# Kernel tuning notes

Measured on AMD Instinct MI355X. Metric: run time of the kernel, lower is better.

## Reference

```python
import jax, jax.numpy as jnp
import numpy as np

NUM_CAMS, BS, NUM_QUERY, MAX_LEN, EMBED_DIMS, NPTS = 6, 1, 40000, 10000, 256, 4


def setup_inputs() -> dict:
    key = jax.random.key(0)
    kq, kr, km = jax.random.split(key, 3)
    query = jax.random.normal(kq, (BS, NUM_QUERY, EMBED_DIMS), dtype=jnp.float32)
    reference_points_cam = jax.random.normal(
        kr, (NUM_CAMS, BS, NUM_QUERY, NPTS, 2), dtype=jnp.float32)
    bev_mask = jax.random.randint(km, (NUM_CAMS, BS, NUM_QUERY, NPTS), 0, 2).astype(jnp.int32)
    return {"query": query, "reference_points_cam": reference_points_cam, "bev_mask": bev_mask}


def reference(query, reference_points_cam, bev_mask):
    # valid[c, q]: query q is seen by camera c (any of the NPTS mask bits set); bs == 1
    valid = (bev_mask > 0).any(-1)            # (cams, bs, Q) bool
    valid0 = valid[:, 0]                      # (cams, Q)

    # Stable stream compaction: valid indices first, in ascending query order.
    order = jnp.argsort(~valid0, axis=-1, stable=True)      # (cams, Q)
    indexes = order[:, :MAX_LEN].astype(jnp.int32)          # (cams, max_len)
    indexes_len = jnp.minimum(valid0.sum(-1), MAX_LEN).astype(jnp.int32)  # (cams,)

    # Padded gather/rebatch; zero out slots beyond each camera's valid count.
    pos_ok = jnp.arange(MAX_LEN)[None, :] < indexes_len[:, None]          # (cams, max_len)
    queries_rebatch = query[0][indexes]                                   # (cams, max_len, E)
    queries_rebatch = jnp.where(pos_ok[:, :, None], queries_rebatch, 0.0)

    ref0 = reference_points_cam[:, 0]                                     # (cams, Q, NPTS, 2)
    reference_points_rebatch = jax.vmap(lambda r, i: r[i])(ref0, indexes) # (cams, max_len, NPTS, 2)
    reference_points_rebatch = jnp.where(
        pos_ok[:, :, None, None], reference_points_rebatch, 0.0)

    # count_norm: 1 / (number of cameras that see each query, clamped to >= 1)
    count = valid.astype(jnp.float32).sum(0)                 # (bs, Q)
    count_norm = (1.0 / jnp.maximum(count, 1.0))[..., None]  # (bs, Q, 1)

    return (indexes,
            indexes_len,
            queries_rebatch.reshape(BS * NUM_CAMS, MAX_LEN, EMBED_DIMS),
            reference_points_rebatch.reshape(BS * NUM_CAMS, MAX_LEN, NPTS, 2),
            count_norm)
```

## Files before the change

kernel.cpp:

```cpp
#include <hip/hip_runtime.h>
#include <hip/hip_bf16.h>

#define NUM_CAMS 6
#define NQ       40000
#define MAX_LEN  10000
#define ED       256
#define NBLK     ((NQ + 255) / 256)

typedef float f32x2 __attribute__((ext_vector_type(2)));

#define OFF_IDX  0
#define OFF_LEN  (NUM_CAMS * MAX_LEN)
#define OFF_Q    (OFF_LEN + NUM_CAMS)
#define OFF_REF  (OFF_Q + NUM_CAMS * MAX_LEN * ED)
#define OFF_CNT  (OFF_REF + NUM_CAMS * MAX_LEN * 8)

#define WS_OFF 0
#define WS_TOT (NUM_CAMS * NBLK)
#define WS_LEN (WS_TOT + NUM_CAMS)
#define WS_POS (WS_LEN + NUM_CAMS + 6)
#define WS_NEED_BYTES ((WS_POS + NUM_CAMS * NQ) * 4)

#define QBLOCKS      (NQ / 4)
#define TAIL_BLOCKS  (NUM_CAMS * MAX_LEN / 4)
#define CNT_BLOCKS   ((NQ + 255) / 256)
#define GATHER_BLOCKS (NUM_CAMS * MAX_LEN / 4)

__global__ void kA_counts(const int* __restrict__ bev, float* __restrict__ out,
                          int* __restrict__ ws) {
    __shared__ int cnt[NUM_CAMS];
    const int tid = threadIdx.x;
    const int blk = blockIdx.x;
    const int q   = blk * 256 + tid;
    if (tid < NUM_CAMS) cnt[tid] = 0;
    __syncthreads();
    const int lane = tid & 63;
    const bool inb = q < NQ;
    int myCount = 0;
    #pragma unroll
    for (int cam = 0; cam < NUM_CAMS; ++cam) {
        bool v = false;
        if (inb) {
            const int4 m = *reinterpret_cast<const int4*>(bev + ((size_t)cam * NQ + q) * 4);
            v = (m.x > 0) | (m.y > 0) | (m.z > 0) | (m.w > 0);
        }
        myCount += v ? 1 : 0;
        unsigned long long bal = __ballot(v);
        if (lane == 0) atomicAdd(&cnt[cam], __popcll(bal));
    }
    if (inb) out[OFF_CNT + q] = 1.0f / fmaxf((float)myCount, 1.0f);
    __syncthreads();
    if (tid < NUM_CAMS) ws[WS_OFF + tid * NBLK + blk] = cnt[tid];
}

__global__ void kB_scan(float* __restrict__ out, int* __restrict__ ws) {
    const int cam  = blockIdx.x;
    const int lane = threadIdx.x;
    int running = 0;
    for (int base = 0; base < NBLK; base += 64) {
        const int i = base + lane;
        int val = (i < NBLK) ? ws[WS_OFF + cam * NBLK + i] : 0;
        int v = val;
        for (int d = 1; d < 64; d <<= 1) {
            int n = __shfl_up(v, d, 64);
            if (lane >= d) v += n;
        }
        if (i < NBLK) ws[WS_OFF + cam * NBLK + i] = v - val + running;
        running += __shfl(v, 63, 64);
    }
    if (lane == 0) {
        ws[WS_TOT + cam] = running;
        const int len = running < MAX_LEN ? running : MAX_LEN;
        ws[WS_LEN + cam] = len;
        out[OFF_LEN + cam] = (float)len;
    }
}

__global__ void kC_indexes(const int* __restrict__ bev, float* __restrict__ out,
                           int* __restrict__ ws, int usePos) {
    const int blk = blockIdx.x;
    const int cam = blockIdx.y;
    const int tid = threadIdx.x;
    const int q    = blk * 256 + tid;
    const int lane = tid & 63;
    const int wave = tid >> 6;
    const bool inb = q < NQ;
    bool v = false;
    if (inb) {
        const int4 m = *reinterpret_cast<const int4*>(bev + ((size_t)cam * NQ + q) * 4);
        v = (m.x > 0) | (m.y > 0) | (m.z > 0) | (m.w > 0);
    }
    const unsigned long long bal = __ballot(v);
    __shared__ int waveSums[4];
    if (lane == 0) waveSums[wave] = __popcll(bal);
    __syncthreads();
    int waveOff = 0;
    #pragma unroll
    for (int w = 0; w < 4; ++w)
        if (w < wave) waveOff += waveSums[w];
    const int prefix   = __popcll(bal & ((1ull << lane) - 1ull));
    const int blockOff = ws[WS_OFF + cam * NBLK + blk];
    const int total    = ws[WS_TOT + cam];
    if (inb) {
        const int vb  = blockOff + waveOff + prefix;
        const int pos = v ? vb : (total + (q - vb));
        if (pos < MAX_LEN) out[OFF_IDX + cam * MAX_LEN + pos] = (float)q;
        if (usePos) ws[WS_POS + cam * NQ + q] = (v && vb < MAX_LEN) ? vb : -1;
    }
}

__global__ void kGatherQ(const float* __restrict__ query, const float* __restrict__ refp,
                         float* __restrict__ out, const int* __restrict__ ws) {
    const int blk   = blockIdx.x;
    const int tid   = threadIdx.x;
    const int group = tid >> 6;
    const int lane  = tid & 63;
    if (blk >= QBLOCKS) {
        const int rowId = (blk - QBLOCKS) * 4 + group;
        const int cam   = rowId / MAX_LEN;
        const int j     = rowId - cam * MAX_LEN;
        if (j < ws[WS_LEN + cam]) return;
        const f32x2 z = (f32x2)(0.f);
        f32x2* o2 = reinterpret_cast<f32x2*>(out + OFF_Q + (size_t)rowId * ED + lane * 4);
        o2[0] = z; o2[1] = z;
        if (lane < 4)
            *reinterpret_cast<f32x2*>(out + OFF_REF + (size_t)rowId * 8 + lane * 2) = z;
        return;
    }
    const int q = blk * 4 + group;

    int pos[NUM_CAMS];
    bool any = false;
    #pragma unroll
    for (int cam = 0; cam < NUM_CAMS; ++cam) {
        const int p = ws[WS_POS + cam * NQ + q];
        pos[cam] = p;
        any |= (p >= 0);
    }
    if (!any) return;

    const float4 vq = *reinterpret_cast<const float4*>(query + (size_t)q * ED + lane * 4);
    f32x2 a; a.x = vq.x; a.y = vq.y;
    f32x2 b; b.x = vq.z; b.y = vq.w;

    #pragma unroll
    for (int cam = 0; cam < NUM_CAMS; ++cam) {
        const int p = pos[cam];
        if (p >= 0) {
            f32x2* o2 = reinterpret_cast<f32x2*>(out + OFF_Q + ((size_t)cam * MAX_LEN + p) * ED + lane * 4);
            __builtin_nontemporal_store(a, o2);
            __builtin_nontemporal_store(b, o2 + 1);
            if (lane < 4) {
                const f32x2 r = *reinterpret_cast<const f32x2*>(refp + ((size_t)cam * NQ + q) * 8 + lane * 2);
                *reinterpret_cast<f32x2*>(out + OFF_REF + ((size_t)cam * MAX_LEN + p) * 8 + lane * 2) = r;
            }
        }
    }
}

__global__ void kGather(const float* __restrict__ query, const float* __restrict__ refp,
                        float* __restrict__ out, const int* __restrict__ ws,
                        const int* __restrict__ bev) {
    const int blk = blockIdx.x;
    const int tid = threadIdx.x;
    if (blk >= GATHER_BLOCKS) {
        const int q = (blk - GATHER_BLOCKS) * 256 + tid;
        if (q < NQ) {
            int cnt = 0;
            #pragma unroll
            for (int cam = 0; cam < NUM_CAMS; ++cam) {
                const int4 m = *reinterpret_cast<const int4*>(bev + ((size_t)cam * NQ + q) * 4);
                cnt += ((m.x > 0) | (m.y > 0) | (m.z > 0) | (m.w > 0)) ? 1 : 0;
            }
            out[OFF_CNT + q] = 1.0f / fmaxf((float)cnt, 1.0f);
        }
        return;
    }
    const int rowId = blk * 4 + (tid >> 6);
    const int lane  = tid & 63;
    const int cam   = rowId / MAX_LEN;
    const int j     = rowId - cam * MAX_LEN;
    const int len   = ws[WS_LEN + cam];

    f32x2 a = (f32x2)(0.f), b = (f32x2)(0.f), r0 = (f32x2)(0.f), r1 = (f32x2)(0.f);
    if (j < len) {
        const int idx = (int)out[OFF_IDX + cam * MAX_LEN + j];
        const float4 vq = *reinterpret_cast<const float4*>(query + (size_t)idx * ED + lane * 4);
        a.x = vq.x; a.y = vq.y;
        b.x = vq.z; b.y = vq.w;
        if (lane < 2) {
            const float4 r = *reinterpret_cast<const float4*>(refp + ((size_t)cam * NQ + idx) * 8 + lane * 4);
            r0.x = r.x; r0.y = r.y;
            r1.x = r.z; r1.y = r.w;
        }
    }
    f32x2* o2 = reinterpret_cast<f32x2*>(out + OFF_Q + (size_t)rowId * ED + lane * 4);
    __builtin_nontemporal_store(a, o2);
    __builtin_nontemporal_store(b, o2 + 1);
    if (lane < 2) {
        f32x2* r2 = reinterpret_cast<f32x2*>(out + OFF_REF + (size_t)rowId * 8 + lane * 4);
        r2[0] = r0;
        r2[1] = r1;
    }
}

extern "C" void kernel_launch(void* const* d_in, const int* in_sizes, int n_in,
                              void* d_out, int out_size, void* d_ws, size_t ws_size,
                              hipStream_t stream) {
    const float* query = (const float*)d_in[0];
    const float* refp  = (const float*)d_in[1];
    const int*   bev   = (const int*)d_in[2];
    float* out = (float*)d_out;
    int*   ws  = (int*)d_ws;
    const int usePos = (ws_size >= (size_t)WS_NEED_BYTES) ? 1 : 0;

    kA_counts<<<NBLK, 256, 0, stream>>>(bev, out, ws);
    kB_scan<<<NUM_CAMS, 64, 0, stream>>>(out, ws);
    kC_indexes<<<dim3(NBLK, NUM_CAMS), 256, 0, stream>>>(bev, out, ws, usePos);
    if (usePos) {
        kGatherQ<<<QBLOCKS + TAIL_BLOCKS, 256, 0, stream>>>(query, refp, out, ws);
    } else {
        kGather<<<GATHER_BLOCKS + CNT_BLOCKS, 256, 0, stream>>>(query, refp, out, ws, bev);
    }
}
```

Baseline: 34.51 us.

## Fuse block-prefix scan into index kernel and drop nontemporal stores

Removes the separate single-wave scan kernel. Each index-compaction block now recomputes its own prefix offset and per-camera total by reducing all NBLK partial counts with wave shuffles and shared memory. This saves one kernel launch and its serial dependency, at the cost of redundant reduction work in every block. It also replaces the nontemporal stores in both gather kernels with ordinary stores.

```diff
diff --git a/kernel.cpp b/kernel.cpp
--- a/kernel.cpp
+++ b/kernel.cpp
@@ -16,9 +16,8 @@
 #define OFF_CNT  (OFF_REF + NUM_CAMS * MAX_LEN * 8)
 
 #define WS_OFF 0
-#define WS_TOT (NUM_CAMS * NBLK)
-#define WS_LEN (WS_TOT + NUM_CAMS)
-#define WS_POS (WS_LEN + NUM_CAMS + 6)
+#define WS_LEN (NUM_CAMS * NBLK)
+#define WS_POS (WS_LEN + NUM_CAMS + 4)
 #define WS_NEED_BYTES ((WS_POS + NUM_CAMS * NQ) * 4)
 
 #define QBLOCKS      (NQ / 4)
@@ -53,37 +52,35 @@
     if (tid < NUM_CAMS) ws[WS_OFF + tid * NBLK + blk] = cnt[tid];
 }
 
-__global__ void kB_scan(float* __restrict__ out, int* __restrict__ ws) {
-    const int cam  = blockIdx.x;
-    const int lane = threadIdx.x;
-    int running = 0;
-    for (int base = 0; base < NBLK; base += 64) {
-        const int i = base + lane;
-        int val = (i < NBLK) ? ws[WS_OFF + cam * NBLK + i] : 0;
-        int v = val;
-        for (int d = 1; d < 64; d <<= 1) {
-            int n = __shfl_up(v, d, 64);
-            if (lane >= d) v += n;
-        }
-        if (i < NBLK) ws[WS_OFF + cam * NBLK + i] = v - val + running;
-        running += __shfl(v, 63, 64);
-    }
-    if (lane == 0) {
-        ws[WS_TOT + cam] = running;
-        const int len = running < MAX_LEN ? running : MAX_LEN;
-        ws[WS_LEN + cam] = len;
-        out[OFF_LEN + cam] = (float)len;
-    }
-}
-
-__global__ void kC_indexes(const int* __restrict__ bev, float* __restrict__ out,
-                           int* __restrict__ ws, int usePos) {
+__global__ void kBC_indexes(const int* __restrict__ bev, float* __restrict__ out,
+                            int* __restrict__ ws, int usePos) {
     const int blk = blockIdx.x;
     const int cam = blockIdx.y;
     const int tid = threadIdx.x;
-    const int q    = blk * 256 + tid;
     const int lane = tid & 63;
     const int wave = tid >> 6;
+
+    const int part = (tid < NBLK) ? ws[WS_OFF + cam * NBLK + tid] : 0;
+    int t = part;
+    int o = (tid < blk) ? part : 0;
+    #pragma unroll
+    for (int d = 1; d < 64; d <<= 1) {
+        t += __shfl_xor(t, d, 64);
+        o += __shfl_xor(o, d, 64);
+    }
+    __shared__ int sT[4], sO[4];
+    if (lane == 0) { sT[wave] = t; sO[wave] = o; }
+    __syncthreads();
+    const int total    = sT[0] + sT[1] + sT[2] + sT[3];
+    const int blockOff = sO[0] + sO[1] + sO[2] + sO[3];
+
+    if (blk == 0 && tid == 0) {
+        const int len = total < MAX_LEN ? total : MAX_LEN;
+        ws[WS_LEN + cam] = len;
+        out[OFF_LEN + cam] = (float)len;
+    }
+
+    const int q   = blk * 256 + tid;
     const bool inb = q < NQ;
     bool v = false;
     if (inb) {
@@ -98,9 +95,7 @@
     #pragma unroll
     for (int w = 0; w < 4; ++w)
         if (w < wave) waveOff += waveSums[w];
-    const int prefix   = __popcll(bal & ((1ull << lane) - 1ull));
-    const int blockOff = ws[WS_OFF + cam * NBLK + blk];
-    const int total    = ws[WS_TOT + cam];
+    const int prefix = __popcll(bal & ((1ull << lane) - 1ull));
     if (inb) {
         const int vb  = blockOff + waveOff + prefix;
         const int pos = v ? vb : (total + (q - vb));
@@ -148,8 +143,8 @@
         const int p = pos[cam];
         if (p >= 0) {
             f32x2* o2 = reinterpret_cast<f32x2*>(out + OFF_Q + ((size_t)cam * MAX_LEN + p) * ED + lane * 4);
-            __builtin_nontemporal_store(a, o2);
-            __builtin_nontemporal_store(b, o2 + 1);
+            o2[0] = a;
+            o2[1] = b;
             if (lane < 4) {
                 const f32x2 r = *reinterpret_cast<const f32x2*>(refp + ((size_t)cam * NQ + q) * 8 + lane * 2);
                 *reinterpret_cast<f32x2*>(out + OFF_REF + ((size_t)cam * MAX_LEN + p) * 8 + lane * 2) = r;
@@ -195,8 +190,8 @@
         }
     }
     f32x2* o2 = reinterpret_cast<f32x2*>(out + OFF_Q + (size_t)rowId * ED + lane * 4);
-    __builtin_nontemporal_store(a, o2);
-    __builtin_nontemporal_store(b, o2 + 1);
+    o2[0] = a;
+    o2[1] = b;
     if (lane < 2) {
         f32x2* r2 = reinterpret_cast<f32x2*>(out + OFF_REF + (size_t)rowId * 8 + lane * 4);
         r2[0] = r0;
@@ -215,8 +210,7 @@
     const int usePos = (ws_size >= (size_t)WS_NEED_BYTES) ? 1 : 0;
 
     kA_counts<<<NBLK, 256, 0, stream>>>(bev, out, ws);
-    kB_scan<<<NUM_CAMS, 64, 0, stream>>>(out, ws);
-    kC_indexes<<<dim3(NBLK, NUM_CAMS), 256, 0, stream>>>(bev, out, ws, usePos);
+    kBC_indexes<<<dim3(NBLK, NUM_CAMS), 256, 0, stream>>>(bev, out, ws, usePos);
     if (usePos) {
         kGatherQ<<<QBLOCKS + TAIL_BLOCKS, 256, 0, stream>>>(query, refp, out, ws);
     } else {
```

Measured after the change: 31.20 us. -9.6%, faster.
